# Performance work log

Hardware: AMD Instinct MI355X
Metric: run time of the kernel (lower is better)

The kernel has to match this reference:

```python
import jax, jax.numpy as jnp
import numpy as np

HEADS = 16
DIM_HEAD = 64
LN_EPS = 1e-5
COS_EPS = 1e-8


def setup_inputs() -> dict:
    key = jax.random.key(0)
    ks = jax.random.split(key, 5)
    dim = 1024
    inner = HEADS * DIM_HEAD
    q = jax.random.normal(ks[0], (4, 1024, dim), dtype=jnp.float32)
    k = jax.random.normal(ks[1], (4, 2048, dim), dtype=jnp.float32)
    v = jax.random.normal(ks[2], (4, 2048, dim), dtype=jnp.float32)
    W_in = jax.random.normal(ks[3], (dim, inner), dtype=jnp.float32) * (1.0 / np.sqrt(dim))
    W_out = jax.random.normal(ks[4], (inner, dim), dtype=jnp.float32) * (1.0 / np.sqrt(inner))
    ln_gamma = jnp.ones((dim,), dtype=jnp.float32)
    ln_beta = jnp.zeros((dim,), dtype=jnp.float32)
    b_out = jnp.zeros((dim,), dtype=jnp.float32)
    return {"q": q, "k": k, "v": v, "ln_gamma": ln_gamma, "ln_beta": ln_beta,
            "W_in": W_in, "W_out": W_out, "b_out": b_out}


def _layernorm(x, gamma, beta):
    mu = jnp.mean(x, axis=-1, keepdims=True)
    var = jnp.mean(jnp.square(x - mu), axis=-1, keepdims=True)  # biased, as torch
    return (x - mu) * jax.lax.rsqrt(var + LN_EPS) * gamma + beta


def _project(t, gamma, beta, W_in):
    # LayerNorm -> Linear(no bias) -> split heads: b n (h d) -> b h n d
    x = _layernorm(t, gamma, beta) @ W_in
    b, n, _ = x.shape
    return x.reshape(b, n, HEADS, DIM_HEAD).transpose(0, 2, 1, 3)


def reference(q, k, v, ln_gamma, ln_beta, W_in, W_out, b_out):
    f_q = _project(q, ln_gamma, ln_beta, W_in)  # [b,h,n,d]
    f_k = _project(k, ln_gamma, ln_beta, W_in)  # [b,h,m,d]
    f_v = _project(v, ln_gamma, ln_beta, W_in)  # [b,h,m,d]
    dots = jnp.einsum('bhnd,bhmd->bhnm', f_q, f_k)
    qn = jnp.linalg.norm(f_q, axis=-1, keepdims=True)          # [b,h,n,1]
    kn = jnp.linalg.norm(f_k, axis=-1, keepdims=True)          # [b,h,m,1]
    attn = dots / (qn * kn.transpose(0, 1, 3, 2) + COS_EPS)    # [b,h,n,m]
    out = jnp.einsum('bhnm,bhmd->bhnd', attn, f_v)             # [b,h,n,d]
    b, h, n, d = out.shape
    out = out.transpose(0, 2, 1, 3).reshape(b, n, h * d)       # b n (h d)
    return out @ W_out + b_out
```

## Files before the change

kernel.cpp:

```cpp
#include <hip/hip_runtime.h>

constexpr int BATCH = 4;
constexpr int SEQQ  = 1024;
constexpr int SEQK  = 2048;
constexpr int DIM   = 1024;
constexpr int NH    = 16;
constexpr int DH    = 64;
constexpr int RQ    = BATCH * SEQQ;
constexpr int RK    = BATCH * SEQK;
constexpr int RTOT  = RQ + 2 * RK;
constexpr int BH    = BATCH * NH;
constexpr int NSLC  = 8;
constexpr float LN_EPS = 1e-5f;

typedef _Float16 f16;
typedef __attribute__((ext_vector_type(8))) _Float16 f16x8;
typedef __attribute__((ext_vector_type(4))) float f32x4;

__device__ __forceinline__ void async16(const void* g, void* l) {
  __builtin_amdgcn_global_load_lds(
      (const __attribute__((address_space(1))) void*)g,
      (__attribute__((address_space(3))) void*)l, 16, 0, 0);
}

__global__ void __launch_bounds__(256) ln_to_f16(
    const float* __restrict__ q, const float* __restrict__ k,
    const float* __restrict__ v, const float* __restrict__ gamma,
    const float* __restrict__ beta, f16* __restrict__ a_h) {
  const int row = blockIdx.x * 4 + (threadIdx.x >> 6);
  const int lane = threadIdx.x & 63;
  const float* src;
  if (row < RQ)            src = q + (size_t)row * DIM;
  else if (row < RQ + RK)  src = k + (size_t)(row - RQ) * DIM;
  else                     src = v + (size_t)(row - RQ - RK) * DIM;
  float4 x[4];
  float s = 0.f, s2 = 0.f;
#pragma unroll
  for (int c = 0; c < 4; c++) {
    x[c] = ((const float4*)src)[c * 64 + lane];
    s  += x[c].x + x[c].y + x[c].z + x[c].w;
    s2 += x[c].x * x[c].x + x[c].y * x[c].y + x[c].z * x[c].z + x[c].w * x[c].w;
  }
#pragma unroll
  for (int off = 1; off < 64; off <<= 1) {
    s  += __shfl_xor(s, off);
    s2 += __shfl_xor(s2, off);
  }
  const float mu = s / DIM;
  const float rs = rsqrtf(s2 / DIM - mu * mu + LN_EPS);
#pragma unroll
  for (int c = 0; c < 4; c++) {
    float4 g = ((const float4*)gamma)[c * 64 + lane];
    float4 b = ((const float4*)beta)[c * 64 + lane];
    union { f16 h[4]; uint2 u; } o;
    o.h[0] = (f16)((x[c].x - mu) * rs * g.x + b.x);
    o.h[1] = (f16)((x[c].y - mu) * rs * g.y + b.y);
    o.h[2] = (f16)((x[c].z - mu) * rs * g.z + b.z);
    o.h[3] = (f16)((x[c].w - mu) * rs * g.w + b.w);
    ((uint2*)(a_h + (size_t)row * DIM))[c * 64 + lane] = o.u;
  }
}

__global__ void __launch_bounds__(256) transpose_f16(
    const float* __restrict__ W0, const float* __restrict__ W1,
    f16* __restrict__ T0, f16* __restrict__ T1) {
  const float* W = blockIdx.z ? W1 : W0;
  f16* T = blockIdx.z ? T1 : T0;
  __shared__ float tile[32][33];
  int tx = threadIdx.x & 31, ty = threadIdx.x >> 5;
  int k0 = blockIdx.x * 32, n0 = blockIdx.y * 32;
#pragma unroll
  for (int i = 0; i < 4; i++)
    tile[ty + 8 * i][tx] = W[(size_t)(k0 + ty + 8 * i) * DIM + n0 + tx];
  __syncthreads();
#pragma unroll
  for (int i = 0; i < 4; i++)
    T[(size_t)(n0 + ty + 8 * i) * DIM + k0 + tx] = (f16)tile[tx][ty + 8 * i];
}

constexpr int PT_A = 320 * 64;
constexpr int PT_B = 256 * 64;

#define STAGE_A(buf, kt) do {                                        \
    const f16* s_ = gA + (size_t)(kt) * 64;                          \
    f16* d_ = AsW + (buf) * PT_A;                                    \
    async16(s_,          d_);                                        \
    async16(s_ +  65536, d_ + 4096);                                 \
    async16(s_ + 131072, d_ + 8192);                                 \
    async16(s_ + 196608, d_ + 12288);                                \
    async16(s_ + 262144, d_ + 16384);                                \
  } while (0)

#define STAGE_B(buf, kt) do {                                        \
    const f16* s_ = gB + (size_t)(kt) * 64;                          \
    f16* d_ = BsW + (buf) * PT_B;                                    \
    async16(s_,          d_);                                        \
    async16(s_ +  65536, d_ + 4096);                                 \
    async16(s_ + 131072, d_ + 8192);                                 \
    async16(s_ + 196608, d_ + 12288);                                \
  } while (0)

#define STAGE_AB(buf, kt) do { STAGE_A(buf, kt); STAGE_B(buf, kt); } while (0)

#define WT9 asm volatile("s_waitcnt vmcnt(9)" ::: "memory")
#define WT0 asm volatile("s_waitcnt vmcnt(0)" ::: "memory")
#define STN ((void)0)

#define HALF(BUF, H)                                                 \
    _Pragma("unroll") for (int j_ = 0; j_ < 4; ++j_)                 \
      bf[j_] = *(const f16x8*)(bB##H + (BUF) * PT_B + j_ * 1024);    \
    _Pragma("unroll") for (int f_ = 0; f_ < 5; ++f_)                 \
      af0[f_] = *(const f16x8*)(aB##H + (BUF) * PT_A + f_ * 1024);   \
    _Pragma("unroll") for (int f_ = 0; f_ < 5; ++f_)                 \
      af1[f_] = *(const f16x8*)(aB##H + (BUF) * PT_A + 5120 +        \
                                f_ * 1024);                          \
    __builtin_amdgcn_s_setprio(1);                                   \
    _Pragma("unroll") for (int f_ = 0; f_ < 5; ++f_)                 \
      _Pragma("unroll") for (int j_ = 0; j_ < 4; ++j_)               \
        acc[f_][j_] = __builtin_amdgcn_mfma_f32_16x16x32_f16(        \
            af0[f_], bf[j_], acc[f_][j_], 0, 0, 0);                  \
    _Pragma("unroll") for (int f_ = 0; f_ < 5; ++f_)                 \
      _Pragma("unroll") for (int j_ = 0; j_ < 4; ++j_)               \
        acc[5 + f_][j_] = __builtin_amdgcn_mfma_f32_16x16x32_f16(    \
            af1[f_], bf[j_], acc[5 + f_][j_], 0, 0, 0);              \
    __builtin_amdgcn_s_setprio(0);

#define PHT(BUF, STG, WT) {                                          \
    STG;                                                             \
    __builtin_amdgcn_sched_barrier(0);                               \
    WT;                                                              \
    __builtin_amdgcn_s_barrier();                                    \
    __builtin_amdgcn_sched_barrier(0);                               \
    HALF(BUF, 0)                                                     \
    HALF(BUF, 1)                                                     \
    __builtin_amdgcn_sched_barrier(0);                               \
    __builtin_amdgcn_s_barrier();                                    \
  }

__global__ void __launch_bounds__(512, 2) proj_gemm(
    const f16* __restrict__ A, const f16* __restrict__ Bt,
    f16* __restrict__ C) {
  __shared__ __align__(16) f16 As[2 * PT_A];
  __shared__ __align__(16) f16 Bs[2 * PT_B];

  const int tid = threadIdx.x;
  const int wid = tid >> 6;
  const int lane = tid & 63;
  const int la15 = lane & 15;

  const int bid = blockIdx.x;
  const int swz = (bid & 7) * 32 + (bid >> 3);
  const int row0 = (swz >> 2) * 320;
  const int col0 = (swz & 3) * 256;

  const int wm = (wid >> 2) * 160;
  const int wn = (wid & 3) * 64;

  const int hs = (tid & 7) ^ ((tid >> 3) & 7);
  const f16* gA = A + (size_t)(row0 + (tid >> 3)) * DIM + (hs >> 2) * 32 +
                  (hs & 3) * 8;
  const f16* gB = Bt + (size_t)(col0 + (tid >> 3)) * DIM + (hs >> 2) * 32 +
                  (hs & 3) * 8;
  f16* AsW = As + wid * 512;
  f16* BsW = Bs + wid * 512;

  const int g = lane >> 4;
  const int r7 = la15 & 7;
  const int cs0 = (g ^ r7) * 8;
  const int cs1 = ((4 + g) ^ r7) * 8;
  const f16* aB0 = As + (wm + la15) * 64 + cs0;
  const f16* aB1 = As + (wm + la15) * 64 + cs1;
  const f16* bB0 = Bs + (wn + la15) * 64 + cs0;
  const f16* bB1 = Bs + (wn + la15) * 64 + cs1;

  f32x4 acc[10][4];
#pragma unroll
  for (int i = 0; i < 10; i++)
#pragma unroll
    for (int j = 0; j < 4; j++) acc[i][j] = (f32x4){0.f, 0.f, 0.f, 0.f};
  f16x8 af0[5], af1[5], bf[4];

  STAGE_AB(0, 0);
  __builtin_amdgcn_sched_barrier(0);
  WT0;
  __builtin_amdgcn_s_barrier();
  __builtin_amdgcn_sched_barrier(0);

#pragma unroll 1
  for (int it = 0; it < 7; ++it) {
    const int t1 = 2 * it + 1, t2 = 2 * it + 2;
    PHT(0, STAGE_AB(1, t1), WT9)
    PHT(1, STAGE_AB(0, t2), WT9)
  }
  PHT(0, STAGE_AB(1, 15), WT9)
  PHT(1, STN,             WT0)

  const int crow = (lane >> 4) * 4;
#pragma unroll
  for (int mh = 0; mh < 2; ++mh)
#pragma unroll
    for (int f = 0; f < 5; ++f) {
      const int m = mh * 5 + f;
      const int rbase = row0 + wm + mh * 80 + f * 16 + crow;
#pragma unroll
      for (int r = 0; r < 4; ++r) {
        float s = acc[m][0][r] * acc[m][0][r] + acc[m][1][r] * acc[m][1][r]
                + acc[m][2][r] * acc[m][2][r] + acc[m][3][r] * acc[m][3][r];
        s += __shfl_xor(s, 1);
        s += __shfl_xor(s, 2);
        s += __shfl_xor(s, 4);
        s += __shfl_xor(s, 8);
        if (rbase + r < RQ + RK) {
          const float inv = rsqrtf(s);
#pragma unroll
          for (int j = 0; j < 4; ++j) acc[m][j][r] *= inv;
        }
      }
    }

  f16* sc = As;
  const int wmi = wid >> 2;
  const int ehalf = tid >> 8;
  const int err = (tid >> 4) & 15;
  const int ecc = tid & 15;
  const f16* rb_l = sc + ehalf * (16 * 264) + err * 264 + ecc * 16;
#pragma unroll
  for (int mh = 0; mh < 2; ++mh)
#pragma unroll
    for (int f = 0; f < 5; ++f) {
      const int m = mh * 5 + f;
#pragma unroll
      for (int j = 0; j < 4; ++j)
#pragma unroll
        for (int r = 0; r < 4; ++r)
          sc[wmi * (16 * 264) + (crow + r) * 264 + wn + j * 16 + la15] =
              (f16)acc[m][j][r];
      __syncthreads();
      f16x8 v0 = *(const f16x8*)(rb_l);
      f16x8 v1 = *(const f16x8*)(rb_l + 8);
      const int grow = row0 + ehalf * 160 + mh * 80 + f * 16 + err;
      f16* Cp = C + (size_t)grow * DIM + col0 + ecc * 16;
      *(f16x8*)(Cp) = v0;
      *(f16x8*)(Cp + 8) = v1;
      if (!(mh == 1 && f == 4)) __syncthreads();
    }
}

template <int MT, bool OUT_F16, bool NORMS, bool BIAS, bool PERB>
__global__ void __launch_bounds__(256) mfma_gemm(
    const f16* __restrict__ A, const f16* __restrict__ Bt,
    void* __restrict__ Cout, const float* __restrict__ bias) {
  constexpr int JT = (MT == 128) ? 4 : 2;
  __shared__ f16 Asl[2][MT * 32];
  __shared__ f16 Bsl[2][128 * 32];
  const int t = threadIdx.x;
  const int wid = t >> 6;
  const int lane = t & 63;
  const int row0 = blockIdx.x * MT;
  const int col0 = blockIdx.y * 128;
  const int wm = (MT == 128) ? (wid >> 1) * 64 : 0;
  const int wn = (MT == 128) ? (wid & 1) * 64 : wid * 32;

  const f16* BtB = PERB ? Bt + (size_t)(row0 >> 10) * DIM * DIM : Bt;

  const int rB = 32 * wid + (lane >> 2);
  const int qB = ((lane & 3) - ((rB >> 1) & 3)) & 3;
  const f16* gB = BtB + (size_t)(col0 + rB) * DIM + qB * 8;
  f16* lB0 = Bsl[0] + 32 * wid * 32;
  f16* lB1 = Bsl[1] + 32 * wid * 32;
  const int rA = (MT == 128 ? 32 : 16) * wid + (lane >> 2);
  const int qA = ((lane & 3) - ((rA >> 1) & 3)) & 3;
  const f16* gA = A + (size_t)(row0 + rA) * DIM + qA * 8;
  f16* lA0 = Asl[0] + (MT == 128 ? 32 : 16) * wid * 32;
  f16* lA1 = Asl[1] + (MT == 128 ? 32 : 16) * wid * 32;

  f32x4 acc[4][JT];
#pragma unroll
  for (int i = 0; i < 4; i++)
#pragma unroll
    for (int j = 0; j < JT; j++) acc[i][j] = (f32x4){0.f, 0.f, 0.f, 0.f};

  const int mrow = lane & 15;
  const int kq_p = (((lane >> 4) + ((lane >> 1) & 3)) & 3) * 8;

  for (int kt = 0; kt < DIM / 64; ++kt) {
    if (kt) __syncthreads();
    const int ko = kt * 64;
    async16(gA + ko,      lA0);
    if (MT == 128) async16(gA + ko + 16 * DIM, lA0 + 512);
    async16(gB + ko,      lB0);
    async16(gB + ko + 16 * DIM, lB0 + 512);
    async16(gA + ko + 32, lA1);
    if (MT == 128) async16(gA + ko + 32 + 16 * DIM, lA1 + 512);
    async16(gB + ko + 32, lB1);
    async16(gB + ko + 32 + 16 * DIM, lB1 + 512);
    __syncthreads();

#pragma unroll
    for (int h = 0; h < 2; ++h) {
      f16x8 af[4], bf[JT];
#pragma unroll
      for (int i = 0; i < 4; i++)
        af[i] = *(const f16x8*)(Asl[h] + (wm + i * 16 + mrow) * 32 + kq_p);
#pragma unroll
      for (int j = 0; j < JT; j++)
        bf[j] = *(const f16x8*)(Bsl[h] + (wn + j * 16 + mrow) * 32 + kq_p);
#pragma unroll
      for (int i = 0; i < 4; i++)
#pragma unroll
        for (int j = 0; j < JT; j++)
          acc[i][j] = __builtin_amdgcn_mfma_f32_16x16x32_f16(af[i], bf[j], acc[i][j], 0, 0, 0);
    }
  }

  if (NORMS && MT == 128) {
    if (row0 < RQ + RK) {
      float sums[4][4];
#pragma unroll
      for (int i = 0; i < 4; i++)
#pragma unroll
        for (int r = 0; r < 4; r++) {
          float s = 0.f;
#pragma unroll
          for (int j = 0; j < JT; j++) s += acc[i][j][r] * acc[i][j][r];
          sums[i][r] = s;
        }
#pragma unroll
      for (int off = 1; off < 16; off <<= 1)
#pragma unroll
        for (int i = 0; i < 4; i++)
#pragma unroll
          for (int r = 0; r < 4; r++)
            sums[i][r] += __shfl_xor(sums[i][r], off);
#pragma unroll
      for (int i = 0; i < 4; i++)
#pragma unroll
        for (int r = 0; r < 4; r++) {
          const float inv = rsqrtf(sums[i][r]);
#pragma unroll
          for (int j = 0; j < JT; j++) acc[i][j][r] *= inv;
        }
    }
  }

  const int ccol = lane & 15;
  const int crow = (lane >> 4) * 4;
  if (OUT_F16) {
    f16* C = (f16*)Cout;
#pragma unroll
    for (int j = 0; j < JT; j++) {
      const int col = col0 + wn + j * 16 + ccol;
#pragma unroll
      for (int i = 0; i < 4; i++) {
        f16* Cp = C + (size_t)(row0 + wm + i * 16 + crow) * DIM + col;
#pragma unroll
        for (int r = 0; r < 4; r++) Cp[(size_t)r * DIM] = (f16)acc[i][j][r];
      }
    }
  } else {
    float* C = (float*)Cout;
#pragma unroll
    for (int j = 0; j < JT; j++) {
      const int col = col0 + wn + j * 16 + ccol;
      float bv = BIAS ? bias[col] : 0.f;
#pragma unroll
      for (int i = 0; i < 4; i++) {
        float* Cp = C + (size_t)(row0 + wm + i * 16 + crow) * DIM + col;
#pragma unroll
        for (int r = 0; r < 4; r++) Cp[(size_t)r * DIM] = acc[i][j][r] + bv;
      }
    }
  }
}

__global__ void __launch_bounds__(256) s_kernel(
    const f16* __restrict__ f, float* __restrict__ S4) {
  const int bh = blockIdx.x;
  const int b = bh >> 4, h = bh & 15;
  const int mbase = blockIdx.y * (SEQK / NSLC);
  const int t = threadIdx.x;
  __shared__ float ks[32][68];
  __shared__ float vs[32][68];
  const int lm   = t >> 3;
  const int lseg = (t & 7) * 8;
  const int d1 = (t & 15) * 4;
  const int d2 = (t >> 4) * 4;
  float acc[4][4] = {{0.f}};
  const f16* fk_base = f + ((size_t)RQ + (size_t)b * SEQK) * DIM + h * DH;
  const f16* fv_base = f + ((size_t)RQ + RK + (size_t)b * SEQK) * DIM + h * DH;

  int m = mbase + lm;
  f16x8 kv = *(const f16x8*)(fk_base + (size_t)m * DIM + lseg);
  f16x8 vv = *(const f16x8*)(fv_base + (size_t)m * DIM + lseg);

  constexpr int SUBS = SEQK / NSLC / 32;
  for (int sub = 0; sub < SUBS; ++sub) {
    __syncthreads();
#pragma unroll
    for (int e = 0; e < 8; e++) {
      ks[lm][lseg + e] = (float)kv[e];
      vs[lm][lseg + e] = (float)vv[e];
    }
    __syncthreads();
    if (sub + 1 < SUBS) {
      m = mbase + (sub + 1) * 32 + lm;
      kv = *(const f16x8*)(fk_base + (size_t)m * DIM + lseg);
      vv = *(const f16x8*)(fv_base + (size_t)m * DIM + lseg);
    }
#pragma unroll
    for (int mm = 0; mm < 32; ++mm) {
      float4 kk = *(const float4*)&ks[mm][d1];
      float4 vv2 = *(const float4*)&vs[mm][d2];
      acc[0][0] = fmaf(kk.x, vv2.x, acc[0][0]);
      acc[0][1] = fmaf(kk.x, vv2.y, acc[0][1]);
      acc[0][2] = fmaf(kk.x, vv2.z, acc[0][2]);
      acc[0][3] = fmaf(kk.x, vv2.w, acc[0][3]);
      acc[1][0] = fmaf(kk.y, vv2.x, acc[1][0]);
      acc[1][1] = fmaf(kk.y, vv2.y, acc[1][1]);
      acc[1][2] = fmaf(kk.y, vv2.z, acc[1][2]);
      acc[1][3] = fmaf(kk.y, vv2.w, acc[1][3]);
      acc[2][0] = fmaf(kk.z, vv2.x, acc[2][0]);
      acc[2][1] = fmaf(kk.z, vv2.y, acc[2][1]);
      acc[2][2] = fmaf(kk.z, vv2.z, acc[2][2]);
      acc[2][3] = fmaf(kk.z, vv2.w, acc[2][3]);
      acc[3][0] = fmaf(kk.w, vv2.x, acc[3][0]);
      acc[3][1] = fmaf(kk.w, vv2.y, acc[3][1]);
      acc[3][2] = fmaf(kk.w, vv2.z, acc[3][2]);
      acc[3][3] = fmaf(kk.w, vv2.w, acc[3][3]);
    }
  }
  float* Sp = S4 + ((size_t)blockIdx.y * BH + bh) * DH * DH;
#pragma unroll
  for (int i = 0; i < 4; i++)
#pragma unroll
    for (int j = 0; j < 4; j++)
      Sp[(d1 + i) * DH + (d2 + j)] = acc[i][j];
}

__global__ void __launch_bounds__(256) s_reduce(
    const float* __restrict__ S4, f16* __restrict__ Sh) {
  const int bh = blockIdx.x;
  const int t = threadIdx.x;
  const size_t base = (size_t)bh * DH * DH + t * 16;
  constexpr size_t STR = (size_t)BH * DH * DH;
#pragma unroll
  for (int c = 0; c < 4; c++) {
    float4 s = {0.f, 0.f, 0.f, 0.f};
#pragma unroll
    for (int p = 0; p < NSLC; p++) {
      float4 sp = *(const float4*)(S4 + base + p * STR + 4 * c);
      s.x += sp.x; s.y += sp.y; s.z += sp.z; s.w += sp.w;
    }
    union { f16 h[4]; uint2 u; } o;
    o.h[0] = (f16)s.x; o.h[1] = (f16)s.y; o.h[2] = (f16)s.z; o.h[3] = (f16)s.w;
    *(uint2*)(Sh + base + 4 * c) = o.u;
  }
}

__global__ void __launch_bounds__(256) m_build(
    const f16* __restrict__ wt_out, const f16* __restrict__ Sh,
    f16* __restrict__ Mt) {
  const int n0 = blockIdx.x * 128;
  const int bh = blockIdx.y;
  const int b = bh >> 4, h = bh & 15;
  __shared__ f16 Asl[128 * 64];
  __shared__ f16 Bsl[64 * 64];
  const int t = threadIdx.x;
  const int wid = t >> 6, lane = t & 63;

  const f16* gA = wt_out + (size_t)(n0 + 32 * wid + (lane >> 3)) * DIM
                  + 64 * h + (lane & 7) * 8;
  f16* lA = Asl + 32 * wid * 64;
  const f16* gB = Sh + (size_t)bh * DH * DH + (16 * wid + (lane >> 3)) * 64
                  + (lane & 7) * 8;
  f16* lB = Bsl + 16 * wid * 64;
#pragma unroll
  for (int o = 0; o < 4; o++) async16(gA + (size_t)(8 * o) * DIM, lA + 8 * o * 64);
  async16(gB, lB);
  async16(gB + 8 * 64, lB + 8 * 64);
  __syncthreads();

  const int wm = (wid >> 1) * 64;
  const int wn = (wid & 1) * 32;
  const int mrow = lane & 15;
  f32x4 acc[4][2];
#pragma unroll
  for (int i = 0; i < 4; i++)
#pragma unroll
    for (int j = 0; j < 2; j++) acc[i][j] = (f32x4){0.f, 0.f, 0.f, 0.f};

#pragma unroll
  for (int kh = 0; kh < 2; kh++) {
    const int kq = kh * 32 + (lane >> 4) * 8;
    f16x8 af[4], bf[2];
#pragma unroll
    for (int i = 0; i < 4; i++)
      af[i] = *(const f16x8*)(Asl + (wm + i * 16 + mrow) * 64 + kq);
#pragma unroll
    for (int j = 0; j < 2; j++)
      bf[j] = *(const f16x8*)(Bsl + (wn + j * 16 + mrow) * 64 + kq);
#pragma unroll
    for (int i = 0; i < 4; i++)
#pragma unroll
      for (int j = 0; j < 2; j++)
        acc[i][j] = __builtin_amdgcn_mfma_f32_16x16x32_f16(af[i], bf[j], acc[i][j], 0, 0, 0);
  }

  const int ccol = lane & 15;
  const int crow = (lane >> 4) * 4;
  f16* Mb = Mt + (size_t)b * DIM * DIM;
#pragma unroll
  for (int j = 0; j < 2; j++) {
    const int col = 64 * h + wn + j * 16 + ccol;
#pragma unroll
    for (int i = 0; i < 4; i++) {
      f16* Mp = Mb + (size_t)(n0 + wm + i * 16 + crow) * DIM + col;
#pragma unroll
      for (int r = 0; r < 4; r++) Mp[(size_t)r * DIM] = (f16)acc[i][j][r];
    }
  }
}

extern "C" void kernel_launch(void* const* d_in, const int* in_sizes, int n_in,
                              void* d_out, int out_size, void* d_ws, size_t ws_size,
                              hipStream_t stream) {
  const float* q     = (const float*)d_in[0];
  const float* k     = (const float*)d_in[1];
  const float* v     = (const float*)d_in[2];
  const float* gamma = (const float*)d_in[3];
  const float* beta  = (const float*)d_in[4];
  const float* W_in  = (const float*)d_in[5];
  const float* W_out = (const float*)d_in[6];
  const float* b_out = (const float*)d_in[7];
  float* out = (float*)d_out;

  char* w = (char*)d_ws;
  f16*   f      = (f16*)w;
  f16*   a_h    = f + (size_t)RTOT * DIM;
  f16*   wt_in  = a_h + (size_t)RTOT * DIM;
  f16*   wt_out = wt_in + (size_t)DIM * DIM;
  f16*   Mt     = wt_out + (size_t)DIM * DIM;
  f16*   Sh     = Mt + (size_t)BATCH * DIM * DIM;
  float* S4     = (float*)(Sh + (size_t)BH * DH * DH);

  ln_to_f16<<<RTOT / 4, 256, 0, stream>>>(q, k, v, gamma, beta, a_h);
  transpose_f16<<<dim3(DIM / 32, DIM / 32, 2), 256, 0, stream>>>(
      W_in, W_out, wt_in, wt_out);

  proj_gemm<<<dim3(256), 512, 0, stream>>>(a_h, wt_in, f);

  s_kernel<<<dim3(BH, NSLC), 256, 0, stream>>>(f, S4);

  s_reduce<<<BH, 256, 0, stream>>>(S4, Sh);

  m_build<<<dim3(DIM / 128, BH), 256, 0, stream>>>(wt_out, Sh, Mt);

  mfma_gemm<64, false, false, true, true>
      <<<dim3(RQ / 64, DIM / 128), 256, 0, stream>>>(f, Mt, out, b_out);
}
```

Before: 231.7 us.

## Split projection GEMM k-tile into four sub-phases interleaving LDS reads with async staging

Restructures the projection GEMM main loop so each k-tile runs as four sub-phases, each issuing its own LDS fragment reads and part of the next tile's global-to-LDS staging before a barrier and a batch of MFMAs. The A and B staging loads are spread over the first two sub-phases, and the vmcnt wait moves to the end of the tile. The goal is to interleave memory and compute more finely and to cut register pressure by keeping one A fragment set instead of two. In exchange it adds twice as many block barriers per tile plus explicit lgkmcnt waits, which may cost more synchronisation than it saves.

```diff
diff --git a/kernel.cpp b/kernel.cpp
--- a/kernel.cpp
+++ b/kernel.cpp
@@ -102,40 +102,44 @@
 
 #define STAGE_AB(buf, kt) do { STAGE_A(buf, kt); STAGE_B(buf, kt); } while (0)
 
-#define WT9 asm volatile("s_waitcnt vmcnt(9)" ::: "memory")
 #define WT0 asm volatile("s_waitcnt vmcnt(0)" ::: "memory")
+#define WTN ((void)0)
 #define STN ((void)0)
 
-#define HALF(BUF, H)                                                 \
+#define RDBF(H, BUF)                                                 \
     _Pragma("unroll") for (int j_ = 0; j_ < 4; ++j_)                 \
-      bf[j_] = *(const f16x8*)(bB##H + (BUF) * PT_B + j_ * 1024);    \
+      bf[j_] = *(const f16x8*)(bB##H + (BUF) * PT_B + j_ * 1024)
+
+#define RDAF(H, MH, BUF)                                             \
     _Pragma("unroll") for (int f_ = 0; f_ < 5; ++f_)                 \
-      af0[f_] = *(const f16x8*)(aB##H + (BUF) * PT_A + f_ * 1024);   \
-    _Pragma("unroll") for (int f_ = 0; f_ < 5; ++f_)                 \
-      af1[f_] = *(const f16x8*)(aB##H + (BUF) * PT_A + 5120 +        \
-                                f_ * 1024);                          \
-    __builtin_amdgcn_s_setprio(1);                                   \
-    _Pragma("unroll") for (int f_ = 0; f_ < 5; ++f_)                 \
-      _Pragma("unroll") for (int j_ = 0; j_ < 4; ++j_)               \
-        acc[f_][j_] = __builtin_amdgcn_mfma_f32_16x16x32_f16(        \
-            af0[f_], bf[j_], acc[f_][j_], 0, 0, 0);                  \
-    _Pragma("unroll") for (int f_ = 0; f_ < 5; ++f_)                 \
-      _Pragma("unroll") for (int j_ = 0; j_ < 4; ++j_)               \
-        acc[5 + f_][j_] = __builtin_amdgcn_mfma_f32_16x16x32_f16(    \
-            af1[f_], bf[j_], acc[5 + f_][j_], 0, 0, 0);              \
-    __builtin_amdgcn_s_setprio(0);
-
-#define PHT(BUF, STG, WT) {                                          \
+      af[f_] = *(const f16x8*)(aB##H + (BUF) * PT_A + (MH) * 5120 +  \
+                               f_ * 1024)
+
+#define SUBPH(RDS, STG, WT, MH)                                      \
+  {                                                                  \
+    RDS;                                                             \
     STG;                                                             \
     __builtin_amdgcn_sched_barrier(0);                               \
     WT;                                                              \
     __builtin_amdgcn_s_barrier();                                    \
     __builtin_amdgcn_sched_barrier(0);                               \
-    HALF(BUF, 0)                                                     \
-    HALF(BUF, 1)                                                     \
+    asm volatile("s_waitcnt lgkmcnt(0)" ::: "memory");               \
+    __builtin_amdgcn_sched_barrier(0);                               \
+    __builtin_amdgcn_s_setprio(1);                                   \
+    _Pragma("unroll") for (int f_ = 0; f_ < 5; ++f_)                 \
+      _Pragma("unroll") for (int j_ = 0; j_ < 4; ++j_)               \
+        acc[(MH) * 5 + f_][j_] = __builtin_amdgcn_mfma_f32_16x16x32_f16( \
+            af[f_], bf[j_], acc[(MH) * 5 + f_][j_], 0, 0, 0);        \
+    __builtin_amdgcn_s_setprio(0);                                   \
     __builtin_amdgcn_sched_barrier(0);                               \
     __builtin_amdgcn_s_barrier();                                    \
   }
+
+#define TILE(BUF, STGA, STGB, WTL)                                   \
+  SUBPH({ RDBF(0, BUF); RDAF(0, 0, BUF); }, STGA, WTN, 0)            \
+  SUBPH({ RDAF(0, 1, BUF); },               STGB, WTN, 1)            \
+  SUBPH({ RDBF(1, BUF); RDAF(1, 0, BUF); }, STN,  WTN, 0)            \
+  SUBPH({ RDAF(1, 1, BUF); },               STN,  WTL, 1)
 
 __global__ void __launch_bounds__(512, 2) proj_gemm(
     const f16* __restrict__ A, const f16* __restrict__ Bt,
@@ -178,7 +182,7 @@
   for (int i = 0; i < 10; i++)
 #pragma unroll
     for (int j = 0; j < 4; j++) acc[i][j] = (f32x4){0.f, 0.f, 0.f, 0.f};
-  f16x8 af0[5], af1[5], bf[4];
+  f16x8 af[5], bf[4];
 
   STAGE_AB(0, 0);
   __builtin_amdgcn_sched_barrier(0);
@@ -189,11 +193,11 @@
 #pragma unroll 1
   for (int it = 0; it < 7; ++it) {
     const int t1 = 2 * it + 1, t2 = 2 * it + 2;
-    PHT(0, STAGE_AB(1, t1), WT9)
-    PHT(1, STAGE_AB(0, t2), WT9)
-  }
-  PHT(0, STAGE_AB(1, 15), WT9)
-  PHT(1, STN,             WT0)
+    TILE(0, STAGE_A(1, t1), STAGE_B(1, t1), WT0)
+    TILE(1, STAGE_A(0, t2), STAGE_B(0, t2), WT0)
+  }
+  TILE(0, STAGE_A(1, 15), STAGE_B(1, 15), WT0)
+  TILE(1, STN, STN, WTN)
 
   const int crow = (lane >> 4) * 4;
 #pragma unroll
```

Measured after the change: 230.1 us. Within noise of the previous version (-0.7%).
